# Performance work log

Hardware: AMD Instinct MI355X
Metric: run time of the kernel (lower is better)

The kernel has to match this reference:

```python
import jax, jax.numpy as jnp
import numpy as np

N, E, D, H = 10000, 160000, 128, 4  # nodes, edges, node/edge dim, heads
HC = H * D  # 512, concat output dim of TransformerConv
LN_EPS = 1e-5


def setup_inputs() -> dict:
    key = jax.random.key(0)
    ks = jax.random.split(key, 16)
    s = 1.0 / np.sqrt(D)
    s2 = 1.0 / np.sqrt(HC)
    return {
        "x": jax.random.normal(ks[0], (N, D), jnp.float32),
        "edge_index": jax.random.randint(ks[1], (2, E), 0, N, jnp.int64),
        "edge_attr": jax.random.normal(ks[2], (E, D), jnp.float32),
        "Wq": jax.random.normal(ks[3], (D, HC), jnp.float32) * s,
        "bq": jnp.zeros((HC,), jnp.float32),
        "Wk": jax.random.normal(ks[4], (D, HC), jnp.float32) * s,
        "bk": jnp.zeros((HC,), jnp.float32),
        "Wv": jax.random.normal(ks[5], (D, HC), jnp.float32) * s,
        "bv": jnp.zeros((HC,), jnp.float32),
        "We": jax.random.normal(ks[6], (D, HC), jnp.float32) * s,
        "be": jnp.zeros((HC,), jnp.float32),
        "Wskip": jax.random.normal(ks[7], (D, HC), jnp.float32) * s,
        "bskip": jnp.zeros((HC,), jnp.float32),
        "ln_g": jnp.ones((HC,), jnp.float32),
        "ln_b": jnp.zeros((HC,), jnp.float32),
        "Wlin": jax.random.normal(ks[8], (HC, D), jnp.float32) * s2,
        "blin": jnp.zeros((D,), jnp.float32),
    }


def reference(x, edge_index, edge_attr, Wq, bq, Wk, bk, Wv, bv, We, be,
              Wskip, bskip, ln_g, ln_b, Wlin, blin):
    n = x.shape[0]
    src, dst = edge_index[0], edge_index[1]  # message flows src -> dst
    q = (x @ Wq + bq).reshape(n, H, D)
    k = (x @ Wk + bk).reshape(n, H, D)
    v = (x @ Wv + bv).reshape(n, H, D)
    e = (edge_attr @ We + be).reshape(-1, H, D)  # [E,H,D]

    kj = k[src] + e                                   # [E,H,D]
    alpha = jnp.einsum('ehd,ehd->eh', q[dst], kj) / np.sqrt(D)  # [E,H]
    # per-destination-node, per-head softmax over incoming edges
    amax = jax.ops.segment_max(alpha, dst, num_segments=n)      # [N,H]
    ex = jnp.exp(alpha - amax[dst])
    denom = jax.ops.segment_sum(ex, dst, num_segments=n)        # [N,H]
    attn = ex / denom[dst]                                      # [E,H]

    msg = (v[src] + e) * attn[:, :, None]                       # [E,H,D]
    agg = jax.ops.segment_sum(msg, dst, num_segments=n).reshape(n, HC)
    out = agg + (x @ Wskip + bskip)  # root/skip connection (concat heads)

    # LayerNorm over H*D
    mu = out.mean(-1, keepdims=True)
    var = ((out - mu) ** 2).mean(-1, keepdims=True)
    normed = (out - mu) * jax.lax.rsqrt(var + LN_EPS) * ln_g + ln_b

    lin = normed @ Wlin + blin
    return jax.nn.elu(lin + x)
```

## Files before the change

kernel.cpp:

```cpp
#include <hip/hip_runtime.h>
#include <math.h>


typedef short bf16x8 __attribute__((ext_vector_type(8)));
typedef unsigned short u16x8 __attribute__((ext_vector_type(8)));
typedef float f32x4 __attribute__((ext_vector_type(4)));

__device__ inline unsigned short f2bf(float f) {
    union { float f; unsigned u; } v; v.f = f;
    unsigned r = (v.u + 0x7FFFu + ((v.u >> 16) & 1u)) >> 16;
    return (unsigned short)r;
}
__device__ inline float bf2f(unsigned short u) {
    union { unsigned u; float f; } v; v.u = ((unsigned)u) << 16; return v.f;
}

__global__ __launch_bounds__(256) void wqe_k(
    const float* __restrict__ Wq, const float* __restrict__ bq,
    const float* __restrict__ We,
    float* __restrict__ WqeT, float* __restrict__ bqe)
{
    const int b = blockIdx.x;
    if (b < 256) {
        const int gid = b * 256 + threadIdx.x;
        const int m = gid >> 9, hc = gid & 511;
        const int h = hc >> 7, c = hc & 127;
        const float* wq = &Wq[(size_t)m * 512 + h * 128];
        const float* we = &We[(size_t)c * 512 + h * 128];
        float s0 = 0.f, s1 = 0.f;
        #pragma unroll 8
        for (int d = 0; d < 128; d += 2) { s0 += wq[d] * we[d]; s1 += wq[d + 1] * we[d + 1]; }
        WqeT[(size_t)m * 512 + hc] = s0 + s1;
    } else {
        const int hc = (b - 256) * 256 + threadIdx.x;
        const int h = hc >> 7, c = hc & 127;
        const float* we = &We[(size_t)c * 512 + h * 128];
        const float* bb = &bq[h * 128];
        float s = 0.f;
        #pragma unroll 8
        for (int d = 0; d < 128; ++d) s += bb[d] * we[d];
        bqe[hc] = s;
    }
}

__global__ __launch_bounds__(256) void prep_k(
    const float* __restrict__ x,
    const float* __restrict__ Wq, const float* __restrict__ bq,
    const float* __restrict__ Wk, const float* __restrict__ bk,
    const float* __restrict__ Wv, const float* __restrict__ bv,
    const float* __restrict__ Ws, const float* __restrict__ bs,
    const float* __restrict__ WqeT, const float* __restrict__ bqe,
    const float* __restrict__ We, const float* __restrict__ Wlin,
    unsigned short* __restrict__ x_bf, unsigned short* __restrict__ Wfrag,
    unsigned short* __restrict__ Wefrag, unsigned short* __restrict__ Wlfrag,
    float* __restrict__ bcat, int n, int nb1)
{
    const int b = blockIdx.x, t = threadIdx.x;
    if (b < nb1) {
        int i = (b * 256 + t) * 4;
        if (i < n * 128) {
            float4 v = *(const float4*)&x[i];
            unsigned short o[4] = { f2bf(v.x), f2bf(v.y), f2bf(v.z), f2bf(v.w) };
            *(uint2*)&x_bf[i] = *(uint2*)o;
        }
    } else if (b < nb1 + 160) {
        int g = (b - nb1) * 256 + t;
        int lane = g & 63, kt = (g >> 6) & 3, nt = g >> 8;
        int ncol = nt * 16 + (lane & 15);
        int k0 = kt * 32 + ((lane >> 4) << 3);
        const float* W; int c;
        if      (ncol < 512)  { W = Wq;   c = ncol; }
        else if (ncol < 1024) { W = Wk;   c = ncol - 512; }
        else if (ncol < 1536) { W = Wv;   c = ncol - 1024; }
        else if (ncol < 2048) { W = Ws;   c = ncol - 1536; }
        else                  { W = WqeT; c = ncol - 2048; }
        unsigned short o[8];
        #pragma unroll
        for (int j = 0; j < 8; ++j) o[j] = f2bf(W[(size_t)(k0 + j) * 512 + c]);
        *(uint4*)&Wfrag[(size_t)g * 8] = *(uint4*)o;
    } else if (b < nb1 + 192) {
        int g = (b - nb1 - 160) * 256 + t;
        int lane = g & 63, kt = (g >> 6) & 3, nt = g >> 8;
        int ncol = nt * 16 + (lane & 15);
        int k0 = kt * 32 + ((lane >> 4) << 3);
        unsigned short o[8];
        #pragma unroll
        for (int j = 0; j < 8; ++j) o[j] = f2bf(We[(size_t)(k0 + j) * 512 + ncol]);
        *(uint4*)&Wefrag[(size_t)g * 8] = *(uint4*)o;
    } else if (b < nb1 + 224) {
        int g = (b - nb1 - 192) * 256 + t;
        int lane = g & 63, kt = (g >> 6) & 15, nt = g >> 10;
        int ncol = nt * 16 + (lane & 15);
        int k0 = kt * 32 + ((lane >> 4) << 3);
        unsigned short o[8];
        #pragma unroll
        for (int j = 0; j < 8; ++j) o[j] = f2bf(Wlin[(size_t)(k0 + j) * 128 + ncol]);
        *(uint4*)&Wlfrag[(size_t)g * 8] = *(uint4*)o;
    } else {
        int c = (b - nb1 - 224) * 256 + t;
        if (c < 2560)
            bcat[c] = (c < 512) ? bq[c] : (c < 1024) ? bk[c - 512] : (c < 1536) ? bv[c - 1024]
                     : (c < 2048) ? bs[c - 1536] : bqe[c - 2048];
    }
}

__global__ __launch_bounds__(256) void node_gemm_mfma(
    const unsigned short* __restrict__ x_bf, const unsigned short* __restrict__ Wfrag,
    const float* __restrict__ bcat, float* __restrict__ qs,
    unsigned short* __restrict__ kvq, int n)
{
    const int t = threadIdx.x, lane = t & 63, w = t >> 6;
    const int m0 = blockIdx.x * 64 + (w >> 1) * 32;
    const int n0 = blockIdx.y * 64 + (w & 1) * 32;
    const int lr = lane & 15, lk = (lane >> 4) << 3;
    f32x4 acc[2][2] = {};
    #pragma unroll
    for (int kt = 0; kt < 4; ++kt) {
        bf16x8 a[2], bf[2];
        #pragma unroll
        for (int mi = 0; mi < 2; ++mi) {
            int row = m0 + mi * 16 + lr; row = row < n ? row : n - 1;
            a[mi] = *(const bf16x8*)&x_bf[(size_t)row * 128 + kt * 32 + lk];
        }
        #pragma unroll
        for (int ni = 0; ni < 2; ++ni) {
            int nt = (n0 + ni * 16) >> 4;
            bf[ni] = *(const bf16x8*)&Wfrag[(size_t)((nt * 4 + kt) * 64 + lane) * 8];
        }
        #pragma unroll
        for (int mi = 0; mi < 2; ++mi)
            #pragma unroll
            for (int ni = 0; ni < 2; ++ni)
                acc[mi][ni] = __builtin_amdgcn_mfma_f32_16x16x32_bf16(a[mi], bf[ni], acc[mi][ni], 0, 0, 0);
    }
    #pragma unroll
    for (int mi = 0; mi < 2; ++mi)
        #pragma unroll
        for (int j = 0; j < 4; ++j) {
            int row = m0 + mi * 16 + (lane >> 4) * 4 + j;
            if (row < n) {
                #pragma unroll
                for (int ni = 0; ni < 2; ++ni) {
                    int col = n0 + ni * 16 + lr;
                    float val = acc[mi][ni][j] + bcat[col];
                    if (col < 512)        qs[(size_t)row * 1024 + col] = val;
                    else if (col < 1536)  kvq[(size_t)row * 1536 + col - 512] = f2bf(val);
                    else if (col < 2048)  qs[(size_t)row * 1024 + col - 1024] = val;
                    else                  kvq[(size_t)row * 1536 + col - 1024] = f2bf(val);
                }
            }
        }
}

__global__ void deg_count_k(const int* __restrict__ dst, int* __restrict__ deg, int E)
{
    int e = blockIdx.x * 256 + threadIdx.x;
    if (e < E) atomicAdd(&deg[dst[e]], 1);
}

__global__ __launch_bounds__(1024) void scan_k(const int* __restrict__ deg,
                                               int* __restrict__ row_start,
                                               int* __restrict__ cursor, int n)
{
    __shared__ int part[1024];
    const int t = threadIdx.x;
    const int c0 = t * 16;
    int loc[16];
    int s = 0;
    #pragma unroll
    for (int i = 0; i < 16; ++i) {
        int idx = c0 + i;
        int dv = (idx < n) ? deg[idx] : 0;
        loc[i] = s; s += dv;
    }
    part[t] = s;
    __syncthreads();
    int incl = s;
    for (int off = 1; off < 1024; off <<= 1) {
        int other = (t >= off) ? part[t - off] : 0;
        __syncthreads();
        incl += other;
        part[t] = incl;
        __syncthreads();
    }
    const int base = incl - s;
    #pragma unroll
    for (int i = 0; i < 16; ++i) {
        int idx = c0 + i;
        if (idx < n) { row_start[idx] = base + loc[i]; cursor[idx] = base + loc[i]; }
    }
    if (t == 1023) row_start[n] = incl;
}

__global__ void scatter_k(const int* __restrict__ ei, int* __restrict__ cursor,
                          int2* __restrict__ csr, int E)
{
    int e = blockIdx.x * 256 + threadIdx.x;
    if (e < E) {
        int dnode = ei[E + e];
        int p = atomicAdd(&cursor[dnode], 1);
        csr[p] = make_int2(e, ei[e]);
    }
}

__global__ __launch_bounds__(256) void edge_k(
    const float* __restrict__ qs, const unsigned short* __restrict__ kvq,
    const float* __restrict__ ea, const float* __restrict__ be,
    const int* __restrict__ row_start, const int2* __restrict__ csr,
    unsigned short* __restrict__ wsum_bf, unsigned short* __restrict__ vacc_bf, int n)
{
    const int t = threadIdx.x;
    const int lane = t & 63;
    const int node = blockIdx.x * 4 + (t >> 6);
    if (node >= n) return;
    const int g = lane >> 4;
    const int sl = (lane & 15) * 8;
    const int rs = row_start[node];
    const int deg = row_start[node + 1] - rs;
    const float s = 0.08838834764831845f;

    float q8[8], qe8[8];
    {
        const float* qp = &qs[(size_t)node * 1024 + g * 128 + sl];
        float4 a = *(const float4*)qp, b2 = *(const float4*)(qp + 4);
        q8[0]=a.x*s;  q8[1]=a.y*s;  q8[2]=a.z*s;  q8[3]=a.w*s;
        q8[4]=b2.x*s; q8[5]=b2.y*s; q8[6]=b2.z*s; q8[7]=b2.w*s;
        u16x8 u = *(const u16x8*)&kvq[(size_t)node * 1536 + 1024 + g * 128 + sl];
        #pragma unroll
        for (int i = 0; i < 8; ++i) qe8[i] = bf2f(u[i]) * s;
    }
    float qbe;
    {
        const float* bp = &be[g * 128 + sl];
        float pb = 0.f;
        #pragma unroll
        for (int i = 0; i < 8; ++i) pb += q8[i] * bp[i];
        #pragma unroll
        for (int o = 1; o <= 8; o <<= 1) pb += __shfl_xor(pb, o);
        qbe = pb;
    }

    float m = -3.0e38f, den = 0.f;
    float va[8] = {}, ws[8] = {};

    for (int j0 = 0; j0 < deg; j0 += 64) {
        const int cnt = min(64, deg - j0);
        int2 my = make_int2(0, 0);
        if (lane < cnt) my = csr[rs + j0 + lane];
        for (int jj = 0; jj < cnt; jj += 4) {
            int srcv[4], eidv[4]; bool act[4];
            #pragma unroll
            for (int u = 0; u < 4; ++u) {
                int idx = jj + u;
                act[u] = idx < cnt;
                int li = act[u] ? idx : (cnt - 1);
                eidv[u] = __shfl(my.x, li);
                srcv[u] = __shfl(my.y, li);
            }
            float ef[4][8];
            u16x8 kk[4], vv[4];
            #pragma unroll
            for (int u = 0; u < 4; ++u) {
                const float* ep = &ea[(size_t)eidv[u] * 128 + sl];
                float4 A = *(const float4*)ep, B = *(const float4*)(ep + 4);
                ef[u][0]=A.x; ef[u][1]=A.y; ef[u][2]=A.z; ef[u][3]=A.w;
                ef[u][4]=B.x; ef[u][5]=B.y; ef[u][6]=B.z; ef[u][7]=B.w;
                kk[u] = *(const u16x8*)&kvq[(size_t)srcv[u] * 1536 + g * 128 + sl];
                vv[u] = *(const u16x8*)&kvq[(size_t)srcv[u] * 1536 + 512 + g * 128 + sl];
            }
            float p[4] = {0.f, 0.f, 0.f, 0.f};
            #pragma unroll
            for (int i = 0; i < 8; ++i) {
                p[0] += q8[i] * bf2f(kk[0][i]) + qe8[i] * ef[0][i];
                p[1] += q8[i] * bf2f(kk[1][i]) + qe8[i] * ef[1][i];
                p[2] += q8[i] * bf2f(kk[2][i]) + qe8[i] * ef[2][i];
                p[3] += q8[i] * bf2f(kk[3][i]) + qe8[i] * ef[3][i];
            }
            #pragma unroll
            for (int o = 1; o <= 8; o <<= 1) {
                p[0] += __shfl_xor(p[0], o); p[1] += __shfl_xor(p[1], o);
                p[2] += __shfl_xor(p[2], o); p[3] += __shfl_xor(p[3], o);
            }
            float aval[4];
            #pragma unroll
            for (int u = 0; u < 4; ++u) aval[u] = act[u] ? (p[u] + qbe) : -3.0e38f;
            #pragma unroll
            for (int u = 0; u < 4; ++u) {
                const float a = aval[u];
                if (a > m + 8.f) {
                    const float sc = __expf(m - a);
                    den *= sc;
                    #pragma unroll
                    for (int i = 0; i < 8; ++i) { va[i] *= sc; ws[i] *= sc; }
                    m = a;
                }
                const float wgt = __expf(a - m);
                den += wgt;
                #pragma unroll
                for (int i = 0; i < 8; ++i) { va[i] += wgt * bf2f(vv[u][i]); ws[i] += wgt * ef[u][i]; }
            }
        }
    }

    const float rden = (den > 0.f) ? 1.f / den : 0.f;
    unsigned short vo[8], wo[8];
    #pragma unroll
    for (int i = 0; i < 8; ++i) { vo[i] = f2bf(va[i] * rden); wo[i] = f2bf(ws[i] * rden); }
    *(uint4*)&vacc_bf[(size_t)node * 512 + g * 128 + sl] = *(uint4*)vo;
    *(uint4*)&wsum_bf[(size_t)node * 512 + g * 128 + sl] = *(uint4*)wo;
}

__global__ __launch_bounds__(256) void tail_k(
    const unsigned short* __restrict__ wsum_bf, const unsigned short* __restrict__ Wefrag,
    const float* __restrict__ be, const unsigned short* __restrict__ vacc_bf,
    const float* __restrict__ qs, const int* __restrict__ row_start,
    const unsigned short* __restrict__ Wlfrag, const float* __restrict__ lng,
    const float* __restrict__ lnb, const float* __restrict__ blin,
    const float* __restrict__ x, float* __restrict__ out, int n)
{
    const int t = threadIdx.x, lane = t & 63, w = t >> 6;
    const int r0 = blockIdx.x * 16;
    const int lr = lane & 15, lk = (lane >> 4) << 3;
    __shared__ unsigned short nlds[16][520];
    __shared__ float red_s[4][16], red_q[4][16], mval[16], rval[16];

    f32x4 acc[8] = {};
    #pragma unroll
    for (int kt = 0; kt < 4; ++kt) {
        int row = r0 + lr; row = row < n ? row : n - 1;
        bf16x8 a = *(const bf16x8*)&wsum_bf[(size_t)row * 512 + w * 128 + kt * 32 + lk];
        #pragma unroll
        for (int ni = 0; ni < 8; ++ni) {
            bf16x8 bfr = *(const bf16x8*)&Wefrag[(size_t)(((w * 8 + ni) * 4 + kt) * 64 + lane) * 8];
            acc[ni] = __builtin_amdgcn_mfma_f32_16x16x32_bf16(a, bfr, acc[ni], 0, 0, 0);
        }
    }
    float g8[8], b8[8];
    #pragma unroll
    for (int ni = 0; ni < 8; ++ni) { int col = w * 128 + ni * 16 + lr; g8[ni] = lng[col]; b8[ni] = lnb[col]; }
    float sum_[4], sq_[4];
    #pragma unroll
    for (int j = 0; j < 4; ++j) {
        int row = r0 + (lane >> 4) * 4 + j;
        int rowc = row < n ? row : n - 1;
        const float hb = (row_start[rowc + 1] > row_start[rowc]) ? 1.f : 0.f;
        float s = 0.f, q = 0.f;
        #pragma unroll
        for (int ni = 0; ni < 8; ++ni) {
            int col = w * 128 + ni * 16 + lr;
            float y = acc[ni][j] + bf2f(vacc_bf[(size_t)rowc * 512 + col]) + hb * be[col]
                    + qs[(size_t)rowc * 1024 + 512 + col];
            acc[ni][j] = y;
            s += y; q += y * y;
        }
        sum_[j] = s; sq_[j] = q;
    }
    #pragma unroll
    for (int o = 1; o <= 8; o <<= 1) {
        #pragma unroll
        for (int j = 0; j < 4; ++j) { sum_[j] += __shfl_xor(sum_[j], o); sq_[j] += __shfl_xor(sq_[j], o); }
    }
    if (lr == 0) {
        #pragma unroll
        for (int j = 0; j < 4; ++j) {
            red_s[w][(lane >> 4) * 4 + j] = sum_[j];
            red_q[w][(lane >> 4) * 4 + j] = sq_[j];
        }
    }
    __syncthreads();
    if (t < 16) {
        float S = red_s[0][t] + red_s[1][t] + red_s[2][t] + red_s[3][t];
        float Q = red_q[0][t] + red_q[1][t] + red_q[2][t] + red_q[3][t];
        float mu = S * (1.f / 512.f);
        float var = Q * (1.f / 512.f) - mu * mu;
        mval[t] = mu;
        rval[t] = rsqrtf(fmaxf(var, 0.f) + 1e-5f);
    }
    __syncthreads();
    #pragma unroll
    for (int j = 0; j < 4; ++j) {
        int rowl = (lane >> 4) * 4 + j;
        float mu = mval[rowl], rv = rval[rowl];
        #pragma unroll
        for (int ni = 0; ni < 8; ++ni) {
            int col = w * 128 + ni * 16 + lr;
            nlds[rowl][col] = f2bf((acc[ni][j] - mu) * rv * g8[ni] + b8[ni]);
        }
    }
    __syncthreads();
    f32x4 acc2[2] = {};
    #pragma unroll
    for (int kt = 0; kt < 16; ++kt) {
        bf16x8 a2 = *(const bf16x8*)&nlds[lr][kt * 32 + lk];
        #pragma unroll
        for (int ni = 0; ni < 2; ++ni) {
            bf16x8 bfr = *(const bf16x8*)&Wlfrag[(size_t)(((w * 2 + ni) * 16 + kt) * 64 + lane) * 8];
            acc2[ni] = __builtin_amdgcn_mfma_f32_16x16x32_bf16(a2, bfr, acc2[ni], 0, 0, 0);
        }
    }
    #pragma unroll
    for (int j = 0; j < 4; ++j) {
        int row = r0 + (lane >> 4) * 4 + j;
        if (row < n) {
            #pragma unroll
            for (int ni = 0; ni < 2; ++ni) {
                int col = w * 32 + ni * 16 + lr;
                float z = acc2[ni][j] + blin[col] + x[(size_t)row * 128 + col];
                out[(size_t)row * 128 + col] = z > 0.f ? z : expm1f(z);
            }
        }
    }
}

extern "C" void kernel_launch(void* const* d_in, const int* in_sizes, int n_in,
                              void* d_out, int out_size, void* d_ws, size_t ws_size,
                              hipStream_t stream)
{
    const float* x   = (const float*)d_in[0];
    const int*   ei  = (const int*)d_in[1];
    const float* ea  = (const float*)d_in[2];
    const float* Wq  = (const float*)d_in[3];
    const float* bq  = (const float*)d_in[4];
    const float* Wk  = (const float*)d_in[5];
    const float* bk  = (const float*)d_in[6];
    const float* Wv  = (const float*)d_in[7];
    const float* bv  = (const float*)d_in[8];
    const float* We  = (const float*)d_in[9];
    const float* be  = (const float*)d_in[10];
    const float* Wsk = (const float*)d_in[11];
    const float* bsk = (const float*)d_in[12];
    const float* lng = (const float*)d_in[13];
    const float* lnb = (const float*)d_in[14];
    const float* Wl  = (const float*)d_in[15];
    const float* bl  = (const float*)d_in[16];
    float* out = (float*)d_out;

    const int n = in_sizes[0] / 128;
    const int E = in_sizes[1] / 2;

    float* qs    = (float*)d_ws;
    float* WqeT  = qs + (size_t)n * 1024;
    float* bqe   = WqeT + 128 * 512;
    float* bcat  = bqe + 512;
    unsigned short* x_bf    = (unsigned short*)(bcat + 2560);
    unsigned short* wsum_bf = x_bf + (size_t)n * 128;
    unsigned short* vacc_bf = wsum_bf + (size_t)n * 512;
    unsigned short* kvq     = vacc_bf + (size_t)n * 512;
    unsigned short* Wfrag   = kvq + (size_t)n * 1536;
    unsigned short* Wefrag  = Wfrag + 128 * 2560;
    unsigned short* Wlfrag  = Wefrag + 128 * 512;
    int2* csr = (int2*)(((uintptr_t)(Wlfrag + 512 * 128) + 7) & ~(uintptr_t)7);
    int* deg       = (int*)(csr + E);
    int* row_start = deg + n;
    int* cursor    = row_start + n + 1;

    hipMemsetAsync(deg, 0, (size_t)n * sizeof(int), stream);

    wqe_k<<<258, 256, 0, stream>>>(Wq, bq, We, WqeT, bqe);
    const int nb1 = (n * 32 + 255) / 256;
    prep_k<<<nb1 + 234, 256, 0, stream>>>(x, Wq, bq, Wk, bk, Wv, bv, Wsk, bsk, WqeT, bqe,
                                          We, Wl, x_bf, Wfrag, Wefrag, Wlfrag, bcat, n, nb1);
    dim3 g1((n + 63) / 64, 40);
    node_gemm_mfma<<<g1, 256, 0, stream>>>(x_bf, Wfrag, bcat, qs, kvq, n);
    deg_count_k<<<(E + 255) / 256, 256, 0, stream>>>(ei + E, deg, E);
    scan_k<<<1, 1024, 0, stream>>>(deg, row_start, cursor, n);
    scatter_k<<<(E + 255) / 256, 256, 0, stream>>>(ei, cursor, csr, E);
    edge_k<<<(n + 3) / 4, 256, 0, stream>>>(qs, kvq, ea, be, row_start, csr,
                                            wsum_bf, vacc_bf, n);
    tail_k<<<(n + 15) / 16, 256, 0, stream>>>(wsum_bf, Wefrag, be, vacc_bf, qs, row_start,
                                              Wlfrag, lng, lnb, bl, x, out, n);
}
```

Before: 196.1 us.

## Split each node's edges across two waves and store scaled q in bf16

The edge kernel now assigns two waves to each destination node. Each wave runs an online softmax over half of the incoming edges, and the two partial max, denominator and accumulator sets are merged through shared memory. The 1/sqrt(D) scale is folded into Wq, bq and the Wq·We projection, so q is written as bf16 next to k, v and qe instead of as fp32, which cuts per-node q traffic. The inner loop processes two edges per step instead of four, which lowers register pressure. In exchange it adds a block-wide sync, LDS traffic, and slightly lower q precision.

```diff
diff --git a/kernel.cpp b/kernel.cpp
--- a/kernel.cpp
+++ b/kernel.cpp
@@ -5,6 +5,8 @@
 typedef short bf16x8 __attribute__((ext_vector_type(8)));
 typedef unsigned short u16x8 __attribute__((ext_vector_type(8)));
 typedef float f32x4 __attribute__((ext_vector_type(4)));
+
+#define SCALE 0.08838834764831845f
 
 __device__ inline unsigned short f2bf(float f) {
     union { float f; unsigned u; } v; v.f = f;
@@ -30,7 +32,7 @@
         float s0 = 0.f, s1 = 0.f;
         #pragma unroll 8
         for (int d = 0; d < 128; d += 2) { s0 += wq[d] * we[d]; s1 += wq[d + 1] * we[d + 1]; }
-        WqeT[(size_t)m * 512 + hc] = s0 + s1;
+        WqeT[(size_t)m * 512 + hc] = (s0 + s1) * SCALE;
     } else {
         const int hc = (b - 256) * 256 + threadIdx.x;
         const int h = hc >> 7, c = hc & 127;
@@ -39,7 +41,7 @@
         float s = 0.f;
         #pragma unroll 8
         for (int d = 0; d < 128; ++d) s += bb[d] * we[d];
-        bqe[hc] = s;
+        bqe[hc] = s * SCALE;
     }
 }
 
@@ -68,15 +70,15 @@
         int lane = g & 63, kt = (g >> 6) & 3, nt = g >> 8;
         int ncol = nt * 16 + (lane & 15);
         int k0 = kt * 32 + ((lane >> 4) << 3);
-        const float* W; int c;
-        if      (ncol < 512)  { W = Wq;   c = ncol; }
+        const float* W; int c; float sc = 1.f;
+        if      (ncol < 512)  { W = Wq;   c = ncol; sc = SCALE; }
         else if (ncol < 1024) { W = Wk;   c = ncol - 512; }
         else if (ncol < 1536) { W = Wv;   c = ncol - 1024; }
         else if (ncol < 2048) { W = Ws;   c = ncol - 1536; }
         else                  { W = WqeT; c = ncol - 2048; }
         unsigned short o[8];
         #pragma unroll
-        for (int j = 0; j < 8; ++j) o[j] = f2bf(W[(size_t)(k0 + j) * 512 + c]);
+        for (int j = 0; j < 8; ++j) o[j] = f2bf(W[(size_t)(k0 + j) * 512 + c] * sc);
         *(uint4*)&Wfrag[(size_t)g * 8] = *(uint4*)o;
     } else if (b < nb1 + 192) {
         int g = (b - nb1 - 160) * 256 + t;
@@ -99,8 +101,8 @@
     } else {
         int c = (b - nb1 - 224) * 256 + t;
         if (c < 2560)
-            bcat[c] = (c < 512) ? bq[c] : (c < 1024) ? bk[c - 512] : (c < 1536) ? bv[c - 1024]
-                     : (c < 2048) ? bs[c - 1536] : bqe[c - 2048];
+            bcat[c] = (c < 512) ? bq[c] * SCALE : (c < 1024) ? bk[c - 512]
+                     : (c < 1536) ? bv[c - 1024] : (c < 2048) ? bs[c - 1536] : bqe[c - 2048];
     }
 }
 
@@ -143,10 +145,9 @@
                 for (int ni = 0; ni < 2; ++ni) {
                     int col = n0 + ni * 16 + lr;
                     float val = acc[mi][ni][j] + bcat[col];
-                    if (col < 512)        qs[(size_t)row * 1024 + col] = val;
-                    else if (col < 1536)  kvq[(size_t)row * 1536 + col - 512] = f2bf(val);
-                    else if (col < 2048)  qs[(size_t)row * 1024 + col - 1024] = val;
-                    else                  kvq[(size_t)row * 1536 + col - 1024] = f2bf(val);
+                    if (col < 1536)       kvq[(size_t)row * 2048 + col] = f2bf(val);
+                    else if (col < 2048)  qs[(size_t)row * 512 + col - 1536] = val;
+                    else                  kvq[(size_t)row * 2048 + col - 512] = f2bf(val);
                 }
             }
         }
@@ -204,30 +205,35 @@
 }
 
 __global__ __launch_bounds__(256) void edge_k(
-    const float* __restrict__ qs, const unsigned short* __restrict__ kvq,
-    const float* __restrict__ ea, const float* __restrict__ be,
+    const unsigned short* __restrict__ kvq, const float* __restrict__ ea,
+    const float* __restrict__ be,
     const int* __restrict__ row_start, const int2* __restrict__ csr,
     unsigned short* __restrict__ wsum_bf, unsigned short* __restrict__ vacc_bf, int n)
 {
-    const int t = threadIdx.x;
-    const int lane = t & 63;
-    const int node = blockIdx.x * 4 + (t >> 6);
-    if (node >= n) return;
+    const int t = threadIdx.x, lane = t & 63, w = t >> 6;
+    const int slot = w >> 1, half = w & 1;
+    const int node = blockIdx.x * 2 + slot;
+    const bool nvalid = node < n;
+    const int nodec = nvalid ? node : 0;
     const int g = lane >> 4;
-    const int sl = (lane & 15) * 8;
-    const int rs = row_start[node];
-    const int deg = row_start[node + 1] - rs;
-    const float s = 0.08838834764831845f;
+    const int l15 = lane & 15;
+    const int sl = l15 * 8;
+
+    __shared__ float lds_m[2][4], lds_den[2][4];
+    __shared__ float lds_va[2][4][128], lds_ws[2][4][128];
+
+    int rs = 0, deg = 0;
+    if (nvalid) { rs = row_start[node]; deg = row_start[node + 1] - rs; }
+    const int dh = (deg + 1) >> 1;
+    const int lo = half ? dh : 0;
+    const int myc = half ? (deg - dh) : dh;
 
     float q8[8], qe8[8];
     {
-        const float* qp = &qs[(size_t)node * 1024 + g * 128 + sl];
-        float4 a = *(const float4*)qp, b2 = *(const float4*)(qp + 4);
-        q8[0]=a.x*s;  q8[1]=a.y*s;  q8[2]=a.z*s;  q8[3]=a.w*s;
-        q8[4]=b2.x*s; q8[5]=b2.y*s; q8[6]=b2.z*s; q8[7]=b2.w*s;
-        u16x8 u = *(const u16x8*)&kvq[(size_t)node * 1536 + 1024 + g * 128 + sl];
-        #pragma unroll
-        for (int i = 0; i < 8; ++i) qe8[i] = bf2f(u[i]) * s;
+        const u16x8 uq  = *(const u16x8*)&kvq[(size_t)nodec * 2048 + g * 128 + sl];
+        const u16x8 uqe = *(const u16x8*)&kvq[(size_t)nodec * 2048 + 1536 + g * 128 + sl];
+        #pragma unroll
+        for (int i = 0; i < 8; ++i) { q8[i] = bf2f(uq[i]); qe8[i] = bf2f(uqe[i]); }
     }
     float qbe;
     {
@@ -243,71 +249,81 @@
     float m = -3.0e38f, den = 0.f;
     float va[8] = {}, ws[8] = {};
 
-    for (int j0 = 0; j0 < deg; j0 += 64) {
-        const int cnt = min(64, deg - j0);
+    for (int j0 = 0; j0 < myc; j0 += 64) {
+        const int cnt = min(64, myc - j0);
         int2 my = make_int2(0, 0);
-        if (lane < cnt) my = csr[rs + j0 + lane];
-        for (int jj = 0; jj < cnt; jj += 4) {
-            int srcv[4], eidv[4]; bool act[4];
-            #pragma unroll
-            for (int u = 0; u < 4; ++u) {
-                int idx = jj + u;
-                act[u] = idx < cnt;
-                int li = act[u] ? idx : (cnt - 1);
-                eidv[u] = __shfl(my.x, li);
-                srcv[u] = __shfl(my.y, li);
-            }
-            float ef[4][8];
-            u16x8 kk[4], vv[4];
-            #pragma unroll
-            for (int u = 0; u < 4; ++u) {
-                const float* ep = &ea[(size_t)eidv[u] * 128 + sl];
-                float4 A = *(const float4*)ep, B = *(const float4*)(ep + 4);
-                ef[u][0]=A.x; ef[u][1]=A.y; ef[u][2]=A.z; ef[u][3]=A.w;
-                ef[u][4]=B.x; ef[u][5]=B.y; ef[u][6]=B.z; ef[u][7]=B.w;
-                kk[u] = *(const u16x8*)&kvq[(size_t)srcv[u] * 1536 + g * 128 + sl];
-                vv[u] = *(const u16x8*)&kvq[(size_t)srcv[u] * 1536 + 512 + g * 128 + sl];
-            }
-            float p[4] = {0.f, 0.f, 0.f, 0.f};
+        if (lane < cnt) my = csr[rs + lo + j0 + lane];
+        for (int jj = 0; jj < cnt; jj += 2) {
+            const bool two = (jj + 1 < cnt);
+            const int j1 = two ? jj + 1 : jj;
+            const int eid0 = __shfl(my.x, jj), src0 = __shfl(my.y, jj);
+            const int eid1 = __shfl(my.x, j1), src1 = __shfl(my.y, j1);
+            const float* ep0 = &ea[(size_t)eid0 * 128 + sl];
+            const float* ep1 = &ea[(size_t)eid1 * 128 + sl];
+            float4 eA0 = *(const float4*)ep0, eB0 = *(const float4*)(ep0 + 4);
+            float4 eA1 = *(const float4*)ep1, eB1 = *(const float4*)(ep1 + 4);
+            const u16x8 k0 = *(const u16x8*)&kvq[(size_t)src0 * 2048 + 512 + g * 128 + sl];
+            const u16x8 v0 = *(const u16x8*)&kvq[(size_t)src0 * 2048 + 1024 + g * 128 + sl];
+            const u16x8 k1 = *(const u16x8*)&kvq[(size_t)src1 * 2048 + 512 + g * 128 + sl];
+            const u16x8 v1 = *(const u16x8*)&kvq[(size_t)src1 * 2048 + 1024 + g * 128 + sl];
+            float ef0[8] = {eA0.x, eA0.y, eA0.z, eA0.w, eB0.x, eB0.y, eB0.z, eB0.w};
+            float ef1[8] = {eA1.x, eA1.y, eA1.z, eA1.w, eB1.x, eB1.y, eB1.z, eB1.w};
+            float p0 = 0.f, p1 = 0.f;
             #pragma unroll
             for (int i = 0; i < 8; ++i) {
-                p[0] += q8[i] * bf2f(kk[0][i]) + qe8[i] * ef[0][i];
-                p[1] += q8[i] * bf2f(kk[1][i]) + qe8[i] * ef[1][i];
-                p[2] += q8[i] * bf2f(kk[2][i]) + qe8[i] * ef[2][i];
-                p[3] += q8[i] * bf2f(kk[3][i]) + qe8[i] * ef[3][i];
+                p0 += q8[i] * bf2f(k0[i]) + qe8[i] * ef0[i];
+                p1 += q8[i] * bf2f(k1[i]) + qe8[i] * ef1[i];
             }
             #pragma unroll
             for (int o = 1; o <= 8; o <<= 1) {
-                p[0] += __shfl_xor(p[0], o); p[1] += __shfl_xor(p[1], o);
-                p[2] += __shfl_xor(p[2], o); p[3] += __shfl_xor(p[3], o);
-            }
-            float aval[4];
+                p0 += __shfl_xor(p0, o);
+                p1 += __shfl_xor(p1, o);
+            }
+            const float a0 = p0 + qbe;
+            const float a1 = two ? (p1 + qbe) : -3.0e38f;
+            const float gm = fmaxf(a0, a1);
+            if (gm > m + 8.f) {
+                const float sc = __expf(m - gm);
+                den *= sc;
+                #pragma unroll
+                for (int i = 0; i < 8; ++i) { va[i] *= sc; ws[i] *= sc; }
+                m = gm;
+            }
+            const float w0 = __expf(a0 - m);
+            const float w1 = __expf(a1 - m);
+            den += w0 + w1;
             #pragma unroll
-            for (int u = 0; u < 4; ++u) aval[u] = act[u] ? (p[u] + qbe) : -3.0e38f;
-            #pragma unroll
-            for (int u = 0; u < 4; ++u) {
-                const float a = aval[u];
-                if (a > m + 8.f) {
-                    const float sc = __expf(m - a);
-                    den *= sc;
-                    #pragma unroll
-                    for (int i = 0; i < 8; ++i) { va[i] *= sc; ws[i] *= sc; }
-                    m = a;
-                }
-                const float wgt = __expf(a - m);
-                den += wgt;
-                #pragma unroll
-                for (int i = 0; i < 8; ++i) { va[i] += wgt * bf2f(vv[u][i]); ws[i] += wgt * ef[u][i]; }
-            }
-        }
-    }
-
-    const float rden = (den > 0.f) ? 1.f / den : 0.f;
-    unsigned short vo[8], wo[8];
-    #pragma unroll
-    for (int i = 0; i < 8; ++i) { vo[i] = f2bf(va[i] * rden); wo[i] = f2bf(ws[i] * rden); }
-    *(uint4*)&vacc_bf[(size_t)node * 512 + g * 128 + sl] = *(uint4*)vo;
-    *(uint4*)&wsum_bf[(size_t)node * 512 + g * 128 + sl] = *(uint4*)wo;
+            for (int i = 0; i < 8; ++i) {
+                va[i] += w0 * bf2f(v0[i]) + w1 * bf2f(v1[i]);
+                ws[i] += w0 * ef0[i] + w1 * ef1[i];
+            }
+        }
+    }
+
+    if (half == 1) {
+        if (l15 == 0) { lds_m[slot][g] = m; lds_den[slot][g] = den; }
+        #pragma unroll
+        for (int i = 0; i < 8; ++i) {
+            lds_va[slot][g][sl + i] = va[i];
+            lds_ws[slot][g][sl + i] = ws[i];
+        }
+    }
+    __syncthreads();
+    if (half == 0 && nvalid) {
+        const float m1 = lds_m[slot][g], den1 = lds_den[slot][g];
+        const float M = fmaxf(m, m1);
+        const float s0 = __expf(m - M), s1 = __expf(m1 - M);
+        const float dtot = den * s0 + den1 * s1;
+        const float rden = (dtot > 0.f) ? 1.f / dtot : 0.f;
+        unsigned short vo[8], wo[8];
+        #pragma unroll
+        for (int i = 0; i < 8; ++i) {
+            vo[i] = f2bf((va[i] * s0 + lds_va[slot][g][sl + i] * s1) * rden);
+            wo[i] = f2bf((ws[i] * s0 + lds_ws[slot][g][sl + i] * s1) * rden);
+        }
+        *(uint4*)&vacc_bf[(size_t)node * 512 + g * 128 + sl] = *(uint4*)vo;
+        *(uint4*)&wsum_bf[(size_t)node * 512 + g * 128 + sl] = *(uint4*)wo;
+    }
 }
 
 __global__ __launch_bounds__(256) void tail_k(
@@ -349,7 +365,7 @@
         for (int ni = 0; ni < 8; ++ni) {
             int col = w * 128 + ni * 16 + lr;
             float y = acc[ni][j] + bf2f(vacc_bf[(size_t)rowc * 512 + col]) + hb * be[col]
-                    + qs[(size_t)rowc * 1024 + 512 + col];
+                    + qs[(size_t)rowc * 512 + col];
             acc[ni][j] = y;
             s += y; q += y * y;
         }
@@ -439,14 +455,14 @@
     const int E = in_sizes[1] / 2;
 
     float* qs    = (float*)d_ws;
-    float* WqeT  = qs + (size_t)n * 1024;
+    float* WqeT  = qs + (size_t)n * 512;
     float* bqe   = WqeT + 128 * 512;
     float* bcat  = bqe + 512;
     unsigned short* x_bf    = (unsigned short*)(bcat + 2560);
     unsigned short* wsum_bf = x_bf + (size_t)n * 128;
     unsigned short* vacc_bf = wsum_bf + (size_t)n * 512;
     unsigned short* kvq     = vacc_bf + (size_t)n * 512;
-    unsigned short* Wfrag   = kvq + (size_t)n * 1536;
+    unsigned short* Wfrag   = kvq + (size_t)n * 2048;
     unsigned short* Wefrag  = Wfrag + 128 * 2560;
     unsigned short* Wlfrag  = Wefrag + 128 * 512;
     int2* csr = (int2*)(((uintptr_t)(Wlfrag + 512 * 128) + 7) & ~(uintptr_t)7);
@@ -465,7 +481,7 @@
     deg_count_k<<<(E + 255) / 256, 256, 0, stream>>>(ei + E, deg, E);
     scan_k<<<1, 1024, 0, stream>>>(deg, row_start, cursor, n);
     scatter_k<<<(E + 255) / 256, 256, 0, stream>>>(ei, cursor, csr, E);
-    edge_k<<<(n + 3) / 4, 256, 0, stream>>>(qs, kvq, ea, be, row_start, csr,
+    edge_k<<<(n + 1) / 2, 256, 0, stream>>>(kvq, ea, be, row_start, csr,
                                             wsum_bf, vacc_bf, n);
     tail_k<<<(n + 15) / 16, 256, 0, stream>>>(wsum_bf, Wefrag, be, vacc_bf, qs, row_start,
                                               Wlfrag, lng, lnb, bl, x, out, n);
```

Measured after the change: 181.2 us. -7.6%, faster.
